# Optimization experiments

Measured on AMD Instinct MI355X. Metric: run time of the kernel, lower is better.

## Reference

```python
import jax, jax.numpy as jnp
import numpy as np

H = 1024
K = 4  # window_size (causal conv kernel)
HIGHWAY_BIAS = -2.0
SCALE_X = float(np.sqrt(1.0 + np.exp(2.0 * HIGHWAY_BIAS)))  # SRU rescale factor


def _layernorm(x, w, b, eps=1e-5):
    m = jnp.mean(x, axis=-1, keepdims=True)
    v = jnp.mean((x - m) ** 2, axis=-1, keepdims=True)
    return (x - m) * jax.lax.rsqrt(v + eps) * w + b


def _rmsnorm(x, w, eps=1e-6):
    v = jnp.mean(x ** 2, axis=-1, keepdims=True)
    return w * (x * jax.lax.rsqrt(v + eps))


def setup_inputs() -> dict:
    key = jax.random.key(0)
    ks = jax.random.split(key, 12)
    B, L = 8, 4096
    s = 1.0 / np.sqrt(H)
    inp = {
        "x": jax.random.normal(ks[0], (B, L, H), jnp.float32),
        # causal conv1d (full, not depthwise): (out_ch, in_ch, K)
        "conv_w": jax.random.normal(ks[1], (H, H, K), jnp.float32) * (1.0 / np.sqrt(H * K)),
        "conv_b": jnp.zeros((H,), jnp.float32),
        # SRU cell params (k=3 since input_size == hidden_size)
        "sru_ln_w": jnp.ones((H,), jnp.float32),
        "sru_ln_b": jnp.zeros((H,), jnp.float32),
        "sru_W": jax.random.normal(ks[2], (H, 3 * H), jnp.float32) * s,
        "sru_vf": jax.random.normal(ks[3], (H,), jnp.float32) * s,
        "sru_vr": jax.random.normal(ks[4], (H,), jnp.float32) * s,
        "sru_bf": jnp.full((H,), HIGHWAY_BIAS, jnp.float32),
        "sru_br": jnp.zeros((H,), jnp.float32),
        # lambda gate + RMSNorm
        "lambda_w": jax.random.normal(ks[5], (H,), jnp.float32),
        "rms_w": jnp.ones((H,), jnp.float32),
        # FFN token mixer (internal = 2H)
        "ln1_w": jnp.ones((H,), jnp.float32),
        "ln1_b": jnp.zeros((H,), jnp.float32),
        "lin1_w": jax.random.normal(ks[6], (H, 2 * H), jnp.float32) * s,
        "ln2_w": jnp.ones((2 * H,), jnp.float32),
        "ln2_b": jnp.zeros((2 * H,), jnp.float32),
        "lin2_w": jax.random.normal(ks[7], (2 * H, H), jnp.float32) * (1.0 / np.sqrt(2 * H)),
        "lin2_b": jnp.zeros((H,), jnp.float32),
    }
    return inp


def _forward(x, conv_w, conv_b, sru_ln_w, sru_ln_b, sru_W, sru_vf, sru_vr,
             sru_bf, sru_br, lambda_w, rms_w, ln1_w, ln1_b, lin1_w,
             ln2_w, ln2_b, lin2_w, lin2_b):
    B, L, _ = x.shape
    # --- causal conv1d: left-pad K-1, valid conv ---
    xt = jnp.transpose(x, (0, 2, 1))                      # (B, H, L)
    xt = jnp.pad(xt, ((0, 0), (0, 0), (K - 1, 0)))        # (B, H, L+K-1)
    cnn = jax.lax.conv_general_dilated(
        xt, conv_w, window_strides=(1,), padding="VALID",
        dimension_numbers=("NCH", "OIH", "NCH"))          # (B, H, L)
    cnn = cnn + conv_b[None, :, None]
    cnn = jnp.transpose(cnn, (2, 0, 1))                   # (L, B, H)  time-major

    # --- SRU cell (layer_norm=True, use_tanh, rescale) ---
    xn = _layernorm(cnn, sru_ln_w, sru_ln_b)              # (L, B, H)
    U = xn @ sru_W                                        # (L, B, 3H)
    u0, u1, u2 = jnp.split(U, 3, axis=-1)
    xres = xn * SCALE_X

    def step(c, inputs):
        u0t, u1t, u2t, xrt = inputs
        f = jax.nn.sigmoid(u1t + c * sru_vf + sru_bf)
        c_new = f * c + (1.0 - f) * u0t
        r = jax.nn.sigmoid(u2t + c * sru_vr + sru_br)
        h = r * jnp.tanh(c_new) + (1.0 - r) * xrt
        return c_new, h

    c0 = jnp.zeros((B, x.shape[-1]), x.dtype)
    _, hs = jax.lax.scan(step, c0, (u0, u1, u2, xres))    # hs: (L, B, H)

    # --- lambda-gated blend + RMSNorm ---
    out = lambda_w * cnn + (1.0 - lambda_w) * hs          # (L, B, H)
    out = jnp.transpose(out, (1, 0, 2))                   # (B, L, H)
    out = _rmsnorm(out, rms_w)

    # --- block: gate by input, then FFN residual ---
    out = out * x
    t = _layernorm(out, ln1_w, ln1_b)
    t = jax.nn.gelu(t, approximate=False) @ lin1_w        # (B, L, 2H)
    t = _layernorm(t, ln2_w, ln2_b)
    t = jax.nn.gelu(t, approximate=False) @ lin2_w + lin2_b
    return t + out


def reference(x, conv_w, conv_b, sru_ln_w, sru_ln_b, sru_W, sru_vf, sru_vr,
              sru_bf, sru_br, lambda_w, rms_w, ln1_w, ln1_b, lin1_w,
              ln2_w, ln2_b, lin2_w, lin2_b):
    return _forward(x, conv_w, conv_b, sru_ln_w, sru_ln_b, sru_W, sru_vf,
                    sru_vr, sru_bf, sru_br, lambda_w, rms_w, ln1_w, ln1_b,
                    lin1_w, ln2_w, ln2_b, lin2_w, lin2_b)
```

## Files before the change

kernel.cpp:

```cpp
#include <hip/hip_runtime.h>

typedef unsigned short u16;
typedef short bf16x8 __attribute__((ext_vector_type(8)));
typedef float f32x4 __attribute__((ext_vector_type(4)));
typedef unsigned short u16x8 __attribute__((ext_vector_type(8)));

#define NTOK 32768
#define LC 1024
#define L2LC 10
#define NCH 4
#define MC 8192
#define NFC 4

#define OFF_XB     0ull
#define OFF_CNNB   67108864ull
#define OFF_XNB    134217728ull
#define OFF_U4C    201326592ull
#define OFF_WCT    234881024ull
#define OFF_WSRUT  243269632ull
#define OFF_W1T    249561088ull
#define OFF_W2T    253755392ull
#define OFF_CARRY  257949696ull
#define OFF_P      257982464ull
#define OFF_SCALE  258048000ull
#define OFF_FLAG   258179072ull
#define OFF_ZERO   258179328ull
#define WS_REQ     258183168ull

#define P_CONVB 0
#define P_LNW   1024
#define P_LNB   2048
#define P_VF    3072
#define P_VR    4096
#define P_BF    5120
#define P_BR    6144
#define P_LAM   7168
#define P_RMS   8192
#define P_LN1W  9216
#define P_LN1B  10240
#define P_LIN2B 11264
#define P_LN2W  12288
#define P_LN2B  14336

__device__ __forceinline__ float b2f(u16 u) {
    union { unsigned int i; float f; } v; v.i = ((unsigned int)u) << 16; return v.f;
}
__device__ __forceinline__ u16 f2b(float f) {
    union { float f; unsigned int i; } v; v.f = f;
    unsigned int r = v.i + 0x7fffu + ((v.i >> 16) & 1u);
    return (u16)(r >> 16);
}
__device__ __forceinline__ float ldp(const void* p, size_t i, int fl) {
    return fl ? ((const float*)p)[i] : b2f(((const u16*)p)[i]);
}
__device__ __forceinline__ float gelu_exact(float a) {
    return 0.5f * a * (1.0f + erff(a * 0.70710678118654752f));
}

typedef const __attribute__((address_space(1))) void gas_void;
typedef __attribute__((address_space(3))) void las_void;
__device__ __forceinline__ void gl16(const u16* g, u16* l) {
    __builtin_amdgcn_global_load_lds((gas_void*)g, (las_void*)l, 16, 0, 0);
}

__device__ __forceinline__ int kswz(int row) { return (row + (row >> 3)) & 3; }

__global__ __launch_bounds__(256) void k_fill(float* out, float v) {
    size_t i = ((size_t)blockIdx.x * 256 + threadIdx.x) * 4;
    float4 o; o.x = v; o.y = v; o.z = v; o.w = v;
    *(float4*)(out + i) = o;
}

__global__ void k_detect(const u16* __restrict__ x, int* __restrict__ flag) {
    __shared__ int cnt[4];
    int tid = threadIdx.x;
    int c = 0;
    for (int i = 0; i < 16; ++i) {
        float f = b2f(x[2 * (tid * 16 + i)]);
        if (f != f || fabsf(f) > 1e6f) c++;
    }
    #pragma unroll
    for (int m = 32; m; m >>= 1) c += __shfl_xor(c, m, 64);
    if ((tid & 63) == 0) cnt[tid >> 6] = c;
    __syncthreads();
    if (tid == 0) flag[0] = (cnt[0] + cnt[1] + cnt[2] + cnt[3] > 100) ? 1 : 0;
}

__global__ __launch_bounds__(256) void k_params(const int* __restrict__ flag,
        const void* conv_b, const void* lnw, const void* lnb,
        const void* vf, const void* vr, const void* bf, const void* br,
        const void* lam, const void* rms, const void* ln1w, const void* ln1b,
        const void* lin2b, const void* ln2w, const void* ln2b,
        float* __restrict__ P, float* __restrict__ Z) {
    if (blockIdx.x == 0 && threadIdx.x < 32) Z[threadIdx.x] = 0.0f;
    int idx = blockIdx.x * 256 + threadIdx.x;
    int fl = flag[0];
    int vec = idx >> 10, off = idx & 1023;
    const void* src; size_t so = off;
    switch (vec) {
        case 0: src = conv_b; break;
        case 1: src = lnw; break;
        case 2: src = lnb; break;
        case 3: src = vf; break;
        case 4: src = vr; break;
        case 5: src = bf; break;
        case 6: src = br; break;
        case 7: src = lam; break;
        case 8: src = rms; break;
        case 9: src = ln1w; break;
        case 10: src = ln1b; break;
        case 11: src = lin2b; break;
        case 12: case 13: src = ln2w; so = idx - P_LN2W; break;
        default: src = ln2b; so = idx - P_LN2B; break;
    }
    P[idx] = ldp(src, so, fl);
}

__global__ __launch_bounds__(256) void k_x2b(const int* __restrict__ flag,
                                             const void* __restrict__ x, u16* __restrict__ xb) {
    size_t i = (size_t)blockIdx.x * 256 + threadIdx.x;
    int fl = flag[0];
    ushort4 o;
    if (fl) {
        float4 v = ((const float4*)x)[i];
        o.x = f2b(v.x); o.y = f2b(v.y); o.z = f2b(v.z); o.w = f2b(v.w);
    } else {
        o = ((const ushort4*)x)[i];
    }
    ((ushort4*)xb)[i] = o;
}

__global__ __launch_bounds__(256) void k_conv_reorder(const int* __restrict__ flag,
                                                      const void* __restrict__ w, u16* __restrict__ out) {
    int o = blockIdx.x, fl = flag[0];
    for (int kk = threadIdx.x; kk < 4096; kk += 256) {
        int k = kk >> 10, i = kk & 1023;
        out[(size_t)o * 4096 + kk] = f2b(ldp(w, (size_t)o * 4096 + i * 4 + k, fl));
    }
}

__global__ __launch_bounds__(256) void k_transpose(const int* __restrict__ flag,
                                                   const void* __restrict__ in, u16* __restrict__ out,
                                                   int R, int C) {
    int n = blockIdx.x, fl = flag[0];
    for (int r = threadIdx.x; r < R; r += 256)
        out[(size_t)n * R + r] = f2b(ldp(in, (size_t)r * C + n, fl));
}

template<int MODE, int EPI>
__global__ __launch_bounds__(256) void k_gemm(const u16* __restrict__ A, const u16* __restrict__ Bt,
                                              int N, int K, int nn, int l0, int tok0,
                                              const float* __restrict__ P,
                                              const u16* __restrict__ blend,
                                              const void* __restrict__ xorig,
                                              const float* __restrict__ scale,
                                              const int* __restrict__ flag,
                                              const u16* __restrict__ zb,
                                              void* __restrict__ outp) {
    __shared__ __align__(16) u16 As[128 * 32];
    __shared__ __align__(16) u16 Bs[128 * 32];
    const int tid = threadIdx.x;
    const int lane = tid & 63, wid = tid >> 6;
    const int wm = wid >> 1, wn = wid & 1;

    const int nwg = gridDim.x, bid = blockIdx.x;
    const int q = nwg >> 3, r = nwg & 7;
    const int xcd = bid & 7, idx = bid >> 3;
    const int swz = idx + (xcd < r ? xcd * (q + 1) : r * (q + 1) + (xcd - r) * q);
    const int mi = swz / nn, ni = swz - mi * nn;
    const int m0 = mi << 7, n0 = ni << 7;

    const u16* pa[2]; const u16* pb[2]; int kmin[2];
    u16 *la[2], *lb[2];
    #pragma unroll
    for (int j = 0; j < 2; ++j) {
        int s = tid + j * 256;
        int row = s >> 2;
        int kg = ((s & 3) ^ kswz(row)) << 3;
        la[j] = As + ((s & ~63) << 3);
        lb[j] = Bs + ((s & ~63) << 3);
        pb[j] = Bt + (size_t)(n0 + row) * K + kg;
        kmin[j] = 0;
        if (MODE == 1) {
            int t = m0 + row, b = t >> 12, l = t & 4095;
            pa[j] = A + (((size_t)(b << 12) + (size_t)(l - 3)) << 10) + kg;
            kmin[j] = (3 - l) << 10;
        } else if (MODE == 2) {
            int rg = m0 + row;
            int token = ((rg >> L2LC) << 12) + l0 + (rg & (LC - 1));
            pa[j] = A + ((size_t)token << 10) + kg;
        } else {
            pa[j] = A + (size_t)(m0 + row) * K + kg;
        }
    }

    f32x4 acc[4][4];
    #pragma unroll
    for (int a = 0; a < 4; ++a)
        #pragma unroll
        for (int b = 0; b < 4; ++b)
            #pragma unroll
            for (int rr = 0; rr < 4; ++rr) acc[a][b][rr] = 0.0f;

    int ra[4], rb[4];
    #pragma unroll
    for (int sm = 0; sm < 4; ++sm) {
        int rowa = wm * 64 + sm * 16 + (lane & 15);
        int rowb = wn * 64 + sm * 16 + (lane & 15);
        ra[sm] = (rowa << 5) + ((((lane >> 4) ^ kswz(rowa)) & 3) << 3);
        rb[sm] = (rowb << 5) + ((((lane >> 4) ^ kswz(rowb)) & 3) << 3);
    }

    const int nkb = K >> 5;
    for (int kb = 0; kb < nkb; ++kb) {
        const int k0 = kb << 5;
        __syncthreads();
        #pragma unroll
        for (int j = 0; j < 2; ++j) {
            const u16* ga = pa[j] + k0;
            if (MODE == 1) ga = (k0 < kmin[j]) ? zb : ga;
            gl16(ga, la[j]);
            gl16(pb[j] + k0, lb[j]);
        }
        __syncthreads();

        bf16x8 af[4], bfr[4];
        #pragma unroll
        for (int sm = 0; sm < 4; ++sm) af[sm] = *(const bf16x8*)(As + ra[sm]);
        #pragma unroll
        for (int sn = 0; sn < 4; ++sn) bfr[sn] = *(const bf16x8*)(Bs + rb[sn]);
        #pragma unroll
        for (int sm = 0; sm < 4; ++sm)
            #pragma unroll
            for (int sn = 0; sn < 4; ++sn)
                acc[sm][sn] = __builtin_amdgcn_mfma_f32_16x16x32_bf16(af[sm], bfr[sn], acc[sm][sn], 0, 0, 0);
    }

    int fl = 0;
    if (EPI == 3) fl = flag[0];
    #pragma unroll
    for (int sm = 0; sm < 4; ++sm) {
        #pragma unroll
        for (int sn = 0; sn < 4; ++sn) {
            int rbase = m0 + wm * 64 + sm * 16 + ((lane >> 4) * 4);
            int col   = n0 + wn * 64 + sn * 16 + (lane & 15);
            if (EPI == 2) {
                int bI = rbase >> L2LC, rloc = rbase & (LC - 1);
                int p = col >> 10, hh = col & 1023;
                size_t idx8 = ((((size_t)(bI * 3 + p) * (LC / 8)) + (rloc >> 3)) << 10) + hh;
                ushort4 o4;
                o4.x = f2b(acc[sm][sn][0]); o4.y = f2b(acc[sm][sn][1]);
                o4.z = f2b(acc[sm][sn][2]); o4.w = f2b(acc[sm][sn][3]);
                *(ushort4*)((u16*)outp + (idx8 << 3) + (rloc & 7)) = o4;
            } else {
                #pragma unroll
                for (int rr = 0; rr < 4; ++rr) {
                    int rowg = rbase + rr;
                    float v = acc[sm][sn][rr];
                    if (EPI == 0) {
                        ((u16*)outp)[(size_t)rowg * N + col] = f2b(v);
                    } else if (EPI == 1) {
                        ((u16*)outp)[(size_t)rowg * N + col] = f2b(v + P[P_CONVB + col]);
                    } else {
                        size_t gi = ((size_t)(tok0 + rowg) << 10) + col;
                        float xv = ldp(xorig, gi, fl);
                        float g = b2f(blend[gi]) * scale[tok0 + rowg] * P[P_RMS + col] * xv;
                        float o = v + P[P_LIN2B + col] + g;
                        if (fl) ((float*)outp)[gi] = o;
                        else    ((u16*)outp)[gi] = f2b(o);
                    }
                }
            }
        }
    }
}

__device__ __forceinline__ void breduce2(float& a, float& b, volatile float* sa, volatile float* sb, int tid) {
    #pragma unroll
    for (int m = 32; m; m >>= 1) { a += __shfl_xor(a, m, 64); b += __shfl_xor(b, m, 64); }
    int lane = tid & 63, wid = tid >> 6;
    if (lane == 0) { sa[wid] = a; sb[wid] = b; }
    __syncthreads();
    a = sa[0] + sa[1] + sa[2] + sa[3];
    b = sb[0] + sb[1] + sb[2] + sb[3];
    __syncthreads();
}

__global__ __launch_bounds__(256) void k_ln(const u16* __restrict__ cnnb, const float* __restrict__ P,
                                            u16* __restrict__ xnb) {
    __shared__ float sred[8];
    int t = blockIdx.x, tid = threadIdx.x;
    ushort4 cv = ((const ushort4*)(cnnb + ((size_t)t << 10)))[tid];
    float v0 = b2f(cv.x), v1 = b2f(cv.y), v2 = b2f(cv.z), v3 = b2f(cv.w);
    float s = v0 + v1 + v2 + v3;
    float ss = v0 * v0 + v1 * v1 + v2 * v2 + v3 * v3;
    breduce2(s, ss, sred, sred + 4, tid);
    float m = s * (1.0f / 1024.0f);
    float var = ss * (1.0f / 1024.0f) - m * m;
    float rs = rsqrtf(var + 1e-5f);
    int c = tid * 4;
    ushort4 o;
    o.x = f2b((v0 - m) * rs * P[P_LNW + c + 0] + P[P_LNB + c + 0]);
    o.y = f2b((v1 - m) * rs * P[P_LNW + c + 1] + P[P_LNB + c + 1]);
    o.z = f2b((v2 - m) * rs * P[P_LNW + c + 2] + P[P_LNB + c + 2]);
    o.w = f2b((v3 - m) * rs * P[P_LNW + c + 3] + P[P_LNB + c + 3]);
    ((ushort4*)(xnb + ((size_t)t << 10)))[tid] = o;
}

__global__ __launch_bounds__(64) void k_scan(const u16* __restrict__ Uc, const u16* __restrict__ cnnb,
                                             u16* xnblend, float* __restrict__ carry,
                                             const float* __restrict__ P, int l0, int first) {
    int h = blockIdx.x * 64 + threadIdx.x;
    int b = blockIdx.y;
    float vfv = P[P_VF + h], vrv = P[P_VR + h], bfv = P[P_BF + h], brv = P[P_BR + h], lamv = P[P_LAM + h];
    const float SXC = 1.00911627f;
    float c = first ? 0.0f : carry[(b << 10) + h];
    const u16x8* U8 = (const u16x8*)Uc;
    size_t u0b = (((size_t)(b * 3 + 0) * (LC / 8)) << 10) + h;
    size_t u1b = (((size_t)(b * 3 + 1) * (LC / 8)) << 10) + h;
    size_t u2b = (((size_t)(b * 3 + 2) * (LC / 8)) << 10) + h;
    size_t gbase = (((size_t)(b * 4096 + l0)) << 10) + h;

    u16x8 a0[3], a1[3], a2[3];
    u16 bx[3][8], bc[3][8];
    #define SLOAD(g0, s) { \
        size_t gg = (size_t)(g0); \
        a0[s] = U8[u0b + (gg << 10)]; \
        a1[s] = U8[u1b + (gg << 10)]; \
        a2[s] = U8[u2b + (gg << 10)]; \
        _Pragma("unroll") \
        for (int j = 0; j < 8; ++j) { \
            size_t go = gbase + ((gg * 8 + j) << 10); \
            bx[s][j] = xnblend[go]; bc[s][j] = cnnb[go]; \
        } }
    #define SCOMP(g0, s) { \
        _Pragma("unroll") \
        for (int j = 0; j < 8; ++j) { \
            size_t go = gbase + (((size_t)(g0) * 8 + j) << 10); \
            float u0 = b2f(a0[s][j]), u1 = b2f(a1[s][j]), u2 = b2f(a2[s][j]); \
            float xn = b2f(bx[s][j]), cv = b2f(bc[s][j]); \
            float f = 1.0f / (1.0f + __expf(-(u1 + c * vfv + bfv))); \
            float cn = f * (c - u0) + u0; \
            float r_ = 1.0f / (1.0f + __expf(-(u2 + c * vrv + brv))); \
            float e2 = __expf(-2.0f * fabsf(cn)); \
            float th = (1.0f - e2) / (1.0f + e2); \
            th = (cn < 0.0f) ? -th : th; \
            float xr = xn * SXC; \
            float hh = r_ * (th - xr) + xr; \
            xnblend[go] = f2b(lamv * (cv - hh) + hh); \
            c = cn; \
        } }

    const int G = LC / 8;
    SLOAD(0, 0);
    SLOAD(1, 1);
    #pragma unroll 1
    for (int g = 0; g < G; g += 3) {
        if (g + 2 < G) SLOAD(g + 2, 2);
        SCOMP(g, 0);
        if (g + 3 < G) SLOAD(g + 3, 0);
        if (g + 1 < G) SCOMP(g + 1, 1);
        if (g + 4 < G) SLOAD(g + 4, 1);
        if (g + 2 < G) SCOMP(g + 2, 2);
    }
    carry[(b << 10) + h] = c;
    #undef SLOAD
    #undef SCOMP
}

__global__ __launch_bounds__(256) void k_rms_ln1(const u16* __restrict__ blend, const void* __restrict__ x,
                                                 const float* __restrict__ P, const int* __restrict__ flag,
                                                 float* __restrict__ scale, u16* __restrict__ A1) {
    __shared__ float sred[8];
    int t = blockIdx.x, tid = threadIdx.x, fl = flag[0];
    ushort4 bv = ((const ushort4*)(blend + ((size_t)t << 10)))[tid];
    float b0 = b2f(bv.x), b1 = b2f(bv.y), b2 = b2f(bv.z), b3 = b2f(bv.w);
    float ss = b0 * b0 + b1 * b1 + b2 * b2 + b3 * b3, dummy = 0.0f;
    breduce2(ss, dummy, sred, sred + 4, tid);
    float sc = rsqrtf(ss * (1.0f / 1024.0f) + 1e-6f);
    if (tid == 0) scale[t] = sc;
    size_t gb = ((size_t)t << 10) + tid * 4;
    int c = tid * 4;
    float g0 = b0 * sc * P[P_RMS + c + 0] * ldp(x, gb + 0, fl);
    float g1 = b1 * sc * P[P_RMS + c + 1] * ldp(x, gb + 1, fl);
    float g2 = b2 * sc * P[P_RMS + c + 2] * ldp(x, gb + 2, fl);
    float g3 = b3 * sc * P[P_RMS + c + 3] * ldp(x, gb + 3, fl);
    float s2 = g0 + g1 + g2 + g3;
    float ss2 = g0 * g0 + g1 * g1 + g2 * g2 + g3 * g3;
    breduce2(s2, ss2, sred, sred + 4, tid);
    float m = s2 * (1.0f / 1024.0f);
    float var = ss2 * (1.0f / 1024.0f) - m * m;
    float rs = rsqrtf(var + 1e-5f);
    ushort4 o;
    o.x = f2b(gelu_exact((g0 - m) * rs * P[P_LN1W + c + 0] + P[P_LN1B + c + 0]));
    o.y = f2b(gelu_exact((g1 - m) * rs * P[P_LN1W + c + 1] + P[P_LN1B + c + 1]));
    o.z = f2b(gelu_exact((g2 - m) * rs * P[P_LN1W + c + 2] + P[P_LN1B + c + 2]));
    o.w = f2b(gelu_exact((g3 - m) * rs * P[P_LN1W + c + 3] + P[P_LN1B + c + 3]));
    ((ushort4*)(A1 + ((size_t)t << 10)))[tid] = o;
}

__global__ __launch_bounds__(256) void k_ln2_gelu(const u16* __restrict__ T1c, const float* __restrict__ P,
                                                  u16* __restrict__ A2c) {
    __shared__ float sred[8];
    int t = blockIdx.x, tid = threadIdx.x;
    const ushort4* tp = (const ushort4*)(T1c + ((size_t)t << 11));
    ushort4 va = tp[tid * 2], vb = tp[tid * 2 + 1];
    float e[8] = { b2f(va.x), b2f(va.y), b2f(va.z), b2f(va.w),
                   b2f(vb.x), b2f(vb.y), b2f(vb.z), b2f(vb.w) };
    float s = 0.0f, ss = 0.0f;
    #pragma unroll
    for (int i = 0; i < 8; ++i) { s += e[i]; ss += e[i] * e[i]; }
    breduce2(s, ss, sred, sred + 4, tid);
    float m = s * (1.0f / 2048.0f);
    float var = ss * (1.0f / 2048.0f) - m * m;
    float rs = rsqrtf(var + 1e-5f);
    int c = tid * 8;
    u16 oo[8];
    #pragma unroll
    for (int i = 0; i < 8; ++i)
        oo[i] = f2b(gelu_exact((e[i] - m) * rs * P[P_LN2W + c + i] + P[P_LN2B + c + i]));
    ushort4 oa, ob;
    oa.x = oo[0]; oa.y = oo[1]; oa.z = oo[2]; oa.w = oo[3];
    ob.x = oo[4]; ob.y = oo[5]; ob.z = oo[6]; ob.w = oo[7];
    ushort4* op = (ushort4*)(A2c + ((size_t)t << 11));
    op[tid * 2] = oa; op[tid * 2 + 1] = ob;
}

extern "C" void kernel_launch(void* const* d_in, const int* in_sizes, int n_in,
                              void* d_out, int out_size, void* d_ws, size_t ws_size,
                              hipStream_t stream) {
    (void)in_sizes; (void)n_in; (void)out_size;
    const void* x        = d_in[0];
    const void* conv_w   = d_in[1];
    const void* conv_b   = d_in[2];
    const void* sru_ln_w = d_in[3];
    const void* sru_ln_b = d_in[4];
    const void* sru_W    = d_in[5];
    const void* sru_vf   = d_in[6];
    const void* sru_vr   = d_in[7];
    const void* sru_bf   = d_in[8];
    const void* sru_br   = d_in[9];
    const void* lambda_w = d_in[10];
    const void* rms_w    = d_in[11];
    const void* ln1_w    = d_in[12];
    const void* ln1_b    = d_in[13];
    const void* lin1_w   = d_in[14];
    const void* ln2_w    = d_in[15];
    const void* ln2_b    = d_in[16];
    const void* lin2_w   = d_in[17];
    const void* lin2_b   = d_in[18];

    if (ws_size < WS_REQ) {
        float sv = 1000.0f + (float)(ws_size >> 20);
        k_fill<<<16384, 256, 0, stream>>>((float*)d_out, sv);
        return;
    }

    char* ws = (char*)d_ws;
    u16*   xb    = (u16*)(ws + OFF_XB);
    u16*   cnnb  = (u16*)(ws + OFF_CNNB);
    u16*   xnb   = (u16*)(ws + OFF_XNB);
    u16*   Uc    = (u16*)(ws + OFF_XB);
    u16*   WcT   = (u16*)(ws + OFF_WCT);
    u16*   WsruT = (u16*)(ws + OFF_WSRUT);
    u16*   W1T   = (u16*)(ws + OFF_W1T);
    u16*   W2T   = (u16*)(ws + OFF_W2T);
    float* carry = (float*)(ws + OFF_CARRY);
    float* P     = (float*)(ws + OFF_P);
    float* scale = (float*)(ws + OFF_SCALE);
    int*   flag  = (int*)(ws + OFF_FLAG);
    float* zbuf  = (float*)(ws + OFF_ZERO);
    const u16* zb16 = (const u16*)zbuf;
    u16*   A1  = xb;
    u16*   T1c = cnnb;
    u16*   A2c = (u16*)(ws + OFF_CNNB + 33554432);

    k_detect<<<1, 256, 0, stream>>>((const u16*)x, flag);
    k_params<<<64, 256, 0, stream>>>(flag, conv_b, sru_ln_w, sru_ln_b, sru_vf, sru_vr,
                                     sru_bf, sru_br, lambda_w, rms_w, ln1_w, ln1_b,
                                     lin2_b, ln2_w, ln2_b, P, zbuf);
    k_x2b<<<32768, 256, 0, stream>>>(flag, x, xb);
    k_conv_reorder<<<1024, 256, 0, stream>>>(flag, conv_w, WcT);
    k_gemm<1, 1><<<2048, 256, 0, stream>>>(xb, WcT, 1024, 4096, 8, 0, 0,
                                           P, nullptr, nullptr, nullptr, flag, zb16, cnnb);
    k_ln<<<32768, 256, 0, stream>>>(cnnb, P, xnb);
    k_transpose<<<3072, 256, 0, stream>>>(flag, sru_W, WsruT, 1024, 3072);
    for (int ch = 0; ch < NCH; ++ch) {
        int l0 = ch * LC;
        k_gemm<2, 2><<<1536, 256, 0, stream>>>(xnb, WsruT, 3072, 1024, 24, l0, 0,
                                               P, nullptr, nullptr, nullptr, flag, zb16, Uc);
        k_scan<<<dim3(16, 8), 64, 0, stream>>>(Uc, cnnb, xnb, carry, P, l0, ch == 0);
    }
    k_rms_ln1<<<32768, 256, 0, stream>>>(xnb, x, P, flag, scale, A1);
    k_transpose<<<2048, 256, 0, stream>>>(flag, lin1_w, W1T, 1024, 2048);
    k_transpose<<<1024, 256, 0, stream>>>(flag, lin2_w, W2T, 2048, 1024);
    for (int c = 0; c < NFC; ++c) {
        int tok0 = c * MC;
        k_gemm<0, 0><<<1024, 256, 0, stream>>>(A1 + ((size_t)tok0 << 10), W1T, 2048, 1024, 16, 0, 0,
                                               P, nullptr, nullptr, nullptr, flag, zb16, T1c);
        k_ln2_gelu<<<MC, 256, 0, stream>>>(T1c, P, A2c);
        k_gemm<0, 3><<<512, 256, 0, stream>>>(A2c, W2T, 1024, 2048, 8, 0, tok0,
                                              P, xnb, x, scale, flag, zb16, d_out);
    }
}
```

Measured before the change: 2.827 ms.

## Overlap SRU projection GEMM with scan via fused double-buffered kernel

Halves the SRU chunk length and fuses each chunk's U-projection GEMM with the recurrent scan of the previous chunk into one launch, using two U buffers so the latency-bound scan blocks run alongside GEMM tiles. Weight transposes now go through a shared-memory tiled kernel and the conv weight reorder uses vector loads. The FFN second GEMM now processes 16384 tokens per launch, with workspace reassigned to fit. More launches and coupling of scan and GEMM work per kernel add scheduling risk: scan blocks can straggle and set the time of each fused launch.

```diff
diff --git a/kernel.cpp b/kernel.cpp
--- a/kernel.cpp
+++ b/kernel.cpp
@@ -5,14 +5,14 @@
 typedef float f32x4 __attribute__((ext_vector_type(4)));
 typedef unsigned short u16x8 __attribute__((ext_vector_type(8)));
 
-#define NTOK 32768
-#define LC 1024
-#define L2LC 10
-#define NCH 4
+#define LC 512
+#define L2LC 9
+#define LCG 64
+#define NCH 8
 #define MC 8192
-#define NFC 4
 
 #define OFF_XB     0ull
+#define OFF_UCB    25165824ull
 #define OFF_CNNB   67108864ull
 #define OFF_XNB    134217728ull
 #define OFF_U4C    201326592ull
@@ -133,37 +133,58 @@
 __global__ __launch_bounds__(256) void k_conv_reorder(const int* __restrict__ flag,
                                                       const void* __restrict__ w, u16* __restrict__ out) {
     int o = blockIdx.x, fl = flag[0];
-    for (int kk = threadIdx.x; kk < 4096; kk += 256) {
-        int k = kk >> 10, i = kk & 1023;
-        out[(size_t)o * 4096 + kk] = f2b(ldp(w, (size_t)o * 4096 + i * 4 + k, fl));
-    }
-}
-
-__global__ __launch_bounds__(256) void k_transpose(const int* __restrict__ flag,
-                                                   const void* __restrict__ in, u16* __restrict__ out,
-                                                   int R, int C) {
-    int n = blockIdx.x, fl = flag[0];
-    for (int r = threadIdx.x; r < R; r += 256)
-        out[(size_t)n * R + r] = f2b(ldp(in, (size_t)r * C + n, fl));
+    for (int i = threadIdx.x; i < 1024; i += 256) {
+        float f0, f1, f2, f3;
+        if (fl) {
+            float4 v = ((const float4*)w)[(size_t)o * 1024 + i];
+            f0 = v.x; f1 = v.y; f2 = v.z; f3 = v.w;
+        } else {
+            ushort4 v = ((const ushort4*)w)[(size_t)o * 1024 + i];
+            f0 = b2f(v.x); f1 = b2f(v.y); f2 = b2f(v.z); f3 = b2f(v.w);
+        }
+        size_t ob = (size_t)o * 4096 + i;
+        out[ob]        = f2b(f0);
+        out[ob + 1024] = f2b(f1);
+        out[ob + 2048] = f2b(f2);
+        out[ob + 3072] = f2b(f3);
+    }
+}
+
+__global__ __launch_bounds__(256) void k_transpose_t(const int* __restrict__ flag,
+                                                     const void* __restrict__ in, u16* __restrict__ out,
+                                                     int R, int C) {
+    __shared__ float tile[64][65];
+    int fl = flag[0];
+    int c0 = blockIdx.x * 64, r0 = blockIdx.y * 64;
+    int tx = threadIdx.x & 63, ty = threadIdx.x >> 6;
+    #pragma unroll
+    for (int i = 0; i < 16; ++i) {
+        int row = i * 4 + ty;
+        tile[row][tx] = ldp(in, (size_t)(r0 + row) * C + c0 + tx, fl);
+    }
+    __syncthreads();
+    #pragma unroll
+    for (int i = 0; i < 16; ++i) {
+        int col = i * 4 + ty;
+        out[(size_t)(c0 + col) * R + r0 + tx] = f2b(tile[tx][col]);
+    }
 }
 
 template<int MODE, int EPI>
-__global__ __launch_bounds__(256) void k_gemm(const u16* __restrict__ A, const u16* __restrict__ Bt,
-                                              int N, int K, int nn, int l0, int tok0,
-                                              const float* __restrict__ P,
-                                              const u16* __restrict__ blend,
-                                              const void* __restrict__ xorig,
-                                              const float* __restrict__ scale,
-                                              const int* __restrict__ flag,
-                                              const u16* __restrict__ zb,
-                                              void* __restrict__ outp) {
+__device__ __forceinline__ void gemm_core(int bid, int nwg,
+        const u16* __restrict__ A, const u16* __restrict__ Bt,
+        int N, int K, int nn, int l0, int tok0,
+        const float* __restrict__ P, const u16* __restrict__ blend,
+        const void* __restrict__ xorig, const float* __restrict__ scale,
+        const int* __restrict__ flag, const u16* __restrict__ zb,
+        void* __restrict__ outp) {
     __shared__ __align__(16) u16 As[128 * 32];
     __shared__ __align__(16) u16 Bs[128 * 32];
     const int tid = threadIdx.x;
-    const int lane = tid & 63, wid = tid >> 6;
+    const int lane = tid & 63;
+    const int wid = tid >> 6;
     const int wm = wid >> 1, wn = wid & 1;
 
-    const int nwg = gridDim.x, bid = blockIdx.x;
     const int q = nwg >> 3, r = nwg & 7;
     const int xcd = bid & 7, idx = bid >> 3;
     const int swz = idx + (xcd < r ? xcd * (q + 1) : r * (q + 1) + (xcd - r) * q);
@@ -247,7 +268,7 @@
             if (EPI == 2) {
                 int bI = rbase >> L2LC, rloc = rbase & (LC - 1);
                 int p = col >> 10, hh = col & 1023;
-                size_t idx8 = ((((size_t)(bI * 3 + p) * (LC / 8)) + (rloc >> 3)) << 10) + hh;
+                size_t idx8 = ((((size_t)(bI * 3 + p) * LCG) + (rloc >> 3)) << 10) + hh;
                 ushort4 o4;
                 o4.x = f2b(acc[sm][sn][0]); o4.y = f2b(acc[sm][sn][1]);
                 o4.z = f2b(acc[sm][sn][2]); o4.w = f2b(acc[sm][sn][3]);
@@ -275,50 +296,30 @@
     }
 }
 
-__device__ __forceinline__ void breduce2(float& a, float& b, volatile float* sa, volatile float* sb, int tid) {
-    #pragma unroll
-    for (int m = 32; m; m >>= 1) { a += __shfl_xor(a, m, 64); b += __shfl_xor(b, m, 64); }
-    int lane = tid & 63, wid = tid >> 6;
-    if (lane == 0) { sa[wid] = a; sb[wid] = b; }
-    __syncthreads();
-    a = sa[0] + sa[1] + sa[2] + sa[3];
-    b = sb[0] + sb[1] + sb[2] + sb[3];
-    __syncthreads();
-}
-
-__global__ __launch_bounds__(256) void k_ln(const u16* __restrict__ cnnb, const float* __restrict__ P,
-                                            u16* __restrict__ xnb) {
-    __shared__ float sred[8];
-    int t = blockIdx.x, tid = threadIdx.x;
-    ushort4 cv = ((const ushort4*)(cnnb + ((size_t)t << 10)))[tid];
-    float v0 = b2f(cv.x), v1 = b2f(cv.y), v2 = b2f(cv.z), v3 = b2f(cv.w);
-    float s = v0 + v1 + v2 + v3;
-    float ss = v0 * v0 + v1 * v1 + v2 * v2 + v3 * v3;
-    breduce2(s, ss, sred, sred + 4, tid);
-    float m = s * (1.0f / 1024.0f);
-    float var = ss * (1.0f / 1024.0f) - m * m;
-    float rs = rsqrtf(var + 1e-5f);
-    int c = tid * 4;
-    ushort4 o;
-    o.x = f2b((v0 - m) * rs * P[P_LNW + c + 0] + P[P_LNB + c + 0]);
-    o.y = f2b((v1 - m) * rs * P[P_LNW + c + 1] + P[P_LNB + c + 1]);
-    o.z = f2b((v2 - m) * rs * P[P_LNW + c + 2] + P[P_LNB + c + 2]);
-    o.w = f2b((v3 - m) * rs * P[P_LNW + c + 3] + P[P_LNB + c + 3]);
-    ((ushort4*)(xnb + ((size_t)t << 10)))[tid] = o;
-}
-
-__global__ __launch_bounds__(64) void k_scan(const u16* __restrict__ Uc, const u16* __restrict__ cnnb,
-                                             u16* xnblend, float* __restrict__ carry,
-                                             const float* __restrict__ P, int l0, int first) {
-    int h = blockIdx.x * 64 + threadIdx.x;
-    int b = blockIdx.y;
+template<int MODE, int EPI>
+__global__ __launch_bounds__(256) void k_gemm(const u16* __restrict__ A, const u16* __restrict__ Bt,
+                                              int N, int K, int nn, int l0, int tok0,
+                                              const float* __restrict__ P,
+                                              const u16* __restrict__ blend,
+                                              const void* __restrict__ xorig,
+                                              const float* __restrict__ scale,
+                                              const int* __restrict__ flag,
+                                              const u16* __restrict__ zb,
+                                              void* __restrict__ outp) {
+    gemm_core<MODE, EPI>(blockIdx.x, gridDim.x, A, Bt, N, K, nn, l0, tok0,
+                         P, blend, xorig, scale, flag, zb, outp);
+}
+
+__device__ __forceinline__ void scan_core(int h, int b, const u16* __restrict__ Uc,
+        const u16* __restrict__ cnnb, u16* xnblend, float* __restrict__ carry,
+        const float* __restrict__ P, int l0, int first) {
     float vfv = P[P_VF + h], vrv = P[P_VR + h], bfv = P[P_BF + h], brv = P[P_BR + h], lamv = P[P_LAM + h];
     const float SXC = 1.00911627f;
     float c = first ? 0.0f : carry[(b << 10) + h];
     const u16x8* U8 = (const u16x8*)Uc;
-    size_t u0b = (((size_t)(b * 3 + 0) * (LC / 8)) << 10) + h;
-    size_t u1b = (((size_t)(b * 3 + 1) * (LC / 8)) << 10) + h;
-    size_t u2b = (((size_t)(b * 3 + 2) * (LC / 8)) << 10) + h;
+    size_t u0b = (((size_t)(b * 3 + 0) * LCG) << 10) + h;
+    size_t u1b = (((size_t)(b * 3 + 1) * LCG) << 10) + h;
+    size_t u2b = (((size_t)(b * 3 + 2) * LCG) << 10) + h;
     size_t gbase = (((size_t)(b * 4096 + l0)) << 10) + h;
 
     u16x8 a0[3], a1[3], a2[3];
@@ -351,21 +352,74 @@
             c = cn; \
         } }
 
-    const int G = LC / 8;
     SLOAD(0, 0);
     SLOAD(1, 1);
     #pragma unroll 1
-    for (int g = 0; g < G; g += 3) {
-        if (g + 2 < G) SLOAD(g + 2, 2);
+    for (int g = 0; g < LCG; g += 3) {
+        if (g + 2 < LCG) SLOAD(g + 2, 2);
         SCOMP(g, 0);
-        if (g + 3 < G) SLOAD(g + 3, 0);
-        if (g + 1 < G) SCOMP(g + 1, 1);
-        if (g + 4 < G) SLOAD(g + 4, 1);
-        if (g + 2 < G) SCOMP(g + 2, 2);
+        if (g + 3 < LCG) SLOAD(g + 3, 0);
+        if (g + 1 < LCG) SCOMP(g + 1, 1);
+        if (g + 4 < LCG) SLOAD(g + 4, 1);
+        if (g + 2 < LCG) SCOMP(g + 2, 2);
     }
     carry[(b << 10) + h] = c;
     #undef SLOAD
     #undef SCOMP
+}
+
+__global__ __launch_bounds__(256) void k_scan(const u16* __restrict__ Uc, const u16* __restrict__ cnnb,
+                                              u16* xnblend, float* __restrict__ carry,
+                                              const float* __restrict__ P, int l0, int first) {
+    scan_core(blockIdx.x * 256 + threadIdx.x, blockIdx.y, Uc, cnnb, xnblend, carry, P, l0, first);
+}
+
+__global__ __launch_bounds__(256) void k_uscan(const u16* __restrict__ xnb, const u16* __restrict__ WsruT,
+                                               int l0g, u16* __restrict__ UcCur,
+                                               const u16* __restrict__ UcPrev, const u16* __restrict__ cnnb,
+                                               float* __restrict__ carry, int l0s, int first,
+                                               const float* __restrict__ P, const int* __restrict__ flag,
+                                               const u16* __restrict__ zb) {
+    if (blockIdx.x < 32) {
+        int sb = blockIdx.x;
+        scan_core((sb & 3) * 256 + threadIdx.x, sb >> 2, UcPrev, cnnb,
+                  (u16*)xnb, carry, P, l0s, first);
+    } else {
+        gemm_core<2, 2>(blockIdx.x - 32, 768, xnb, WsruT, 3072, 1024, 24, l0g, 0,
+                        P, nullptr, nullptr, nullptr, flag, zb, (void*)UcCur);
+    }
+}
+
+__device__ __forceinline__ void breduce2(float& a, float& b, volatile float* sa, volatile float* sb, int tid) {
+    #pragma unroll
+    for (int m = 32; m; m >>= 1) { a += __shfl_xor(a, m, 64); b += __shfl_xor(b, m, 64); }
+    int lane = tid & 63, wid = tid >> 6;
+    if (lane == 0) { sa[wid] = a; sb[wid] = b; }
+    __syncthreads();
+    a = sa[0] + sa[1] + sa[2] + sa[3];
+    b = sb[0] + sb[1] + sb[2] + sb[3];
+    __syncthreads();
+}
+
+__global__ __launch_bounds__(256) void k_ln(const u16* __restrict__ cnnb, const float* __restrict__ P,
+                                            u16* __restrict__ xnb) {
+    __shared__ float sred[8];
+    int t = blockIdx.x, tid = threadIdx.x;
+    ushort4 cv = ((const ushort4*)(cnnb + ((size_t)t << 10)))[tid];
+    float v0 = b2f(cv.x), v1 = b2f(cv.y), v2 = b2f(cv.z), v3 = b2f(cv.w);
+    float s = v0 + v1 + v2 + v3;
+    float ss = v0 * v0 + v1 * v1 + v2 * v2 + v3 * v3;
+    breduce2(s, ss, sred, sred + 4, tid);
+    float m = s * (1.0f / 1024.0f);
+    float var = ss * (1.0f / 1024.0f) - m * m;
+    float rs = rsqrtf(var + 1e-5f);
+    int c = tid * 4;
+    ushort4 o;
+    o.x = f2b((v0 - m) * rs * P[P_LNW + c + 0] + P[P_LNB + c + 0]);
+    o.y = f2b((v1 - m) * rs * P[P_LNW + c + 1] + P[P_LNB + c + 1]);
+    o.z = f2b((v2 - m) * rs * P[P_LNW + c + 2] + P[P_LNB + c + 2]);
+    o.w = f2b((v3 - m) * rs * P[P_LNW + c + 3] + P[P_LNB + c + 3]);
+    ((ushort4*)(xnb + ((size_t)t << 10)))[tid] = o;
 }
 
 __global__ __launch_bounds__(256) void k_rms_ln1(const u16* __restrict__ blend, const void* __restrict__ x,
@@ -460,7 +514,8 @@
     u16*   xb    = (u16*)(ws + OFF_XB);
     u16*   cnnb  = (u16*)(ws + OFF_CNNB);
     u16*   xnb   = (u16*)(ws + OFF_XNB);
-    u16*   Uc    = (u16*)(ws + OFF_XB);
+    u16*   UcA   = (u16*)(ws + OFF_XB);
+    u16*   UcB   = (u16*)(ws + OFF_UCB);
     u16*   WcT   = (u16*)(ws + OFF_WCT);
     u16*   WsruT = (u16*)(ws + OFF_WSRUT);
     u16*   W1T   = (u16*)(ws + OFF_W1T);
@@ -472,8 +527,8 @@
     float* zbuf  = (float*)(ws + OFF_ZERO);
     const u16* zb16 = (const u16*)zbuf;
     u16*   A1  = xb;
-    u16*   T1c = cnnb;
-    u16*   A2c = (u16*)(ws + OFF_CNNB + 33554432);
+    u16*   T1c = (u16*)(ws + OFF_U4C);
+    u16*   A2  = cnnb;
 
     k_detect<<<1, 256, 0, stream>>>((const u16*)x, flag);
     k_params<<<64, 256, 0, stream>>>(flag, conv_b, sru_ln_w, sru_ln_b, sru_vf, sru_vr,
@@ -484,22 +539,28 @@
     k_gemm<1, 1><<<2048, 256, 0, stream>>>(xb, WcT, 1024, 4096, 8, 0, 0,
                                            P, nullptr, nullptr, nullptr, flag, zb16, cnnb);
     k_ln<<<32768, 256, 0, stream>>>(cnnb, P, xnb);
-    k_transpose<<<3072, 256, 0, stream>>>(flag, sru_W, WsruT, 1024, 3072);
-    for (int ch = 0; ch < NCH; ++ch) {
-        int l0 = ch * LC;
-        k_gemm<2, 2><<<1536, 256, 0, stream>>>(xnb, WsruT, 3072, 1024, 24, l0, 0,
-                                               P, nullptr, nullptr, nullptr, flag, zb16, Uc);
-        k_scan<<<dim3(16, 8), 64, 0, stream>>>(Uc, cnnb, xnb, carry, P, l0, ch == 0);
-    }
+    k_transpose_t<<<dim3(48, 16), 256, 0, stream>>>(flag, sru_W, WsruT, 1024, 3072);
+    k_gemm<2, 2><<<768, 256, 0, stream>>>(xnb, WsruT, 3072, 1024, 24, 0, 0,
+                                          P, nullptr, nullptr, nullptr, flag, zb16, UcA);
+    for (int ch = 1; ch < NCH; ++ch) {
+        u16* cur  = (ch & 1) ? UcB : UcA;
+        u16* prev = (ch & 1) ? UcA : UcB;
+        k_uscan<<<800, 256, 0, stream>>>(xnb, WsruT, ch * LC, cur, prev, cnnb,
+                                         carry, (ch - 1) * LC, ch == 1, P, flag, zb16);
+    }
+    k_scan<<<dim3(4, 8), 256, 0, stream>>>(UcB, cnnb, xnb, carry, P, (NCH - 1) * LC, 0);
     k_rms_ln1<<<32768, 256, 0, stream>>>(xnb, x, P, flag, scale, A1);
-    k_transpose<<<2048, 256, 0, stream>>>(flag, lin1_w, W1T, 1024, 2048);
-    k_transpose<<<1024, 256, 0, stream>>>(flag, lin2_w, W2T, 2048, 1024);
-    for (int c = 0; c < NFC; ++c) {
-        int tok0 = c * MC;
-        k_gemm<0, 0><<<1024, 256, 0, stream>>>(A1 + ((size_t)tok0 << 10), W1T, 2048, 1024, 16, 0, 0,
-                                               P, nullptr, nullptr, nullptr, flag, zb16, T1c);
-        k_ln2_gelu<<<MC, 256, 0, stream>>>(T1c, P, A2c);
-        k_gemm<0, 3><<<512, 256, 0, stream>>>(A2c, W2T, 1024, 2048, 8, 0, tok0,
-                                              P, xnb, x, scale, flag, zb16, d_out);
-    }
-}
+    k_transpose_t<<<dim3(32, 16), 256, 0, stream>>>(flag, lin1_w, W1T, 1024, 2048);
+    k_transpose_t<<<dim3(16, 32), 256, 0, stream>>>(flag, lin2_w, W2T, 2048, 1024);
+    for (int p = 0; p < 2; ++p) {
+        int base = p * 16384;
+        for (int h = 0; h < 2; ++h) {
+            int tok0 = base + h * MC;
+            k_gemm<0, 0><<<1024, 256, 0, stream>>>(A1 + ((size_t)tok0 << 10), W1T, 2048, 1024, 16, 0, 0,
+                                                   P, nullptr, nullptr, nullptr, flag, zb16, T1c);
+            k_ln2_gelu<<<MC, 256, 0, stream>>>(T1c, P, A2 + ((size_t)(h * MC) << 11));
+        }
+        k_gemm<0, 3><<<1024, 256, 0, stream>>>(A2, W2T, 1024, 2048, 8, 0, base,
+                                               P, xnb, x, scale, flag, zb16, d_out);
+    }
+}
```

New measurement: 2.641 ms. 6.6% less time.
